# Optimization experiments

Hardware: AMD Instinct MI355X
Metric: run time of the kernel (lower is better)

## Reference

```python
import jax, jax.numpy as jnp
import numpy as np

B, I, O = 32768, 512, 512
EPS = 1e-5


def setup_inputs() -> dict:
    key = jax.random.key(0)
    ks = jax.random.split(key, 4)
    return {
        "input": jax.random.normal(ks[0], (B, I), dtype=jnp.float32),
        "h": jax.random.normal(ks[1], (B, O), dtype=jnp.float32),
        "c": jax.random.normal(ks[2], (B, O), dtype=jnp.float32),
        "W": jax.random.normal(ks[3], (4 * O, I + O), dtype=jnp.float32) * (1.0 / np.sqrt(I + O)),
        "gamma": jnp.ones((4, O), dtype=jnp.float32),
        "beta": jnp.zeros((4, O), dtype=jnp.float32),
    }


def reference(input, h, c, W, gamma, beta):
    # fused input projection: [B, I+O] @ [I+O, 4O] -> [B, 4, O]
    z = jnp.einsum("bi,gi->bg", jnp.concatenate([input, h], axis=-1), W)
    z = z.reshape(z.shape[0], 4, O)
    # LayerNorm over the trailing [4, O] dims jointly (torch LayerNorm([x, o_size]))
    mean = jnp.mean(z, axis=(-2, -1), keepdims=True)
    var = jnp.var(z, axis=(-2, -1), keepdims=True)
    zn = (z - mean) * jax.lax.rsqrt(var + EPS) * gamma + beta
    f_gate = jax.nn.sigmoid(zn[:, 0])
    i_gate = jax.nn.sigmoid(zn[:, 1])
    o_gate = jax.nn.sigmoid(zn[:, 2])
    # GELU (torch default = exact erf); dropout is identity in eval mode
    h_state = jax.nn.gelu(zn[:, 3], approximate=False)
    cell = f_gate * c + i_gate * h_state
    output = o_gate * cell
    return (output, cell)
```

## Files before the change

kernel.cpp:

```cpp
#include <hip/hip_runtime.h>
#include <hip/hip_bf16.h>
#include <cstdint>
#include <cstddef>

#define BDIM 32768
#define IDIM 512
#define ODIM 512
#define KDIM 1024
#define NDIM 2048

typedef __attribute__((ext_vector_type(8))) __bf16 bf16x8;
typedef __attribute__((ext_vector_type(4))) float f32x4;
typedef __attribute__((ext_vector_type(8))) unsigned short u16x8;

__device__ __forceinline__ unsigned short f2bf(float x) {
  union { float f; uint32_t u; } v; v.f = x;
  uint32_t r = v.u + 0x7FFFu + ((v.u >> 16) & 1u);
  return (unsigned short)(r >> 16);
}

__device__ __forceinline__ float bf2f(unsigned short s) {
  union { uint32_t u; float f; } v; v.u = ((uint32_t)s) << 16;
  return v.f;
}


__global__ __launch_bounds__(256) void pack_a_kernel(const float* __restrict__ in,
                                                     const float* __restrict__ h,
                                                     unsigned short* __restrict__ A) {
  size_t t = (size_t)blockIdx.x * 256 + threadIdx.x;
  size_t e = t * 8;
  size_t b = e >> 10;
  int col = (int)(e & 1023);
  const float* src = (col < IDIM) ? (in + b * IDIM + col)
                                  : (h + b * ODIM + (col - IDIM));
  float4 v0 = ((const float4*)src)[0];
  float4 v1 = ((const float4*)src)[1];
  u16x8 r;
  r[0] = f2bf(v0.x); r[1] = f2bf(v0.y); r[2] = f2bf(v0.z); r[3] = f2bf(v0.w);
  r[4] = f2bf(v1.x); r[5] = f2bf(v1.y); r[6] = f2bf(v1.z); r[7] = f2bf(v1.w);
  *(u16x8*)(A + e) = r;
}

__global__ __launch_bounds__(256) void pack_w_kernel(const float* __restrict__ Wsrc,
                                                     unsigned short* __restrict__ Wb) {
  size_t t = (size_t)blockIdx.x * 256 + threadIdx.x;
  size_t e = t * 8;
  float4 v0 = ((const float4*)(Wsrc + e))[0];
  float4 v1 = ((const float4*)(Wsrc + e))[1];
  u16x8 r;
  r[0] = f2bf(v0.x); r[1] = f2bf(v0.y); r[2] = f2bf(v0.z); r[3] = f2bf(v0.w);
  r[4] = f2bf(v1.x); r[5] = f2bf(v1.y); r[6] = f2bf(v1.z); r[7] = f2bf(v1.w);
  *(u16x8*)(Wb + e) = r;
}


#define GB 65536

#define BAR() do { asm volatile("" ::: "memory"); __builtin_amdgcn_s_barrier(); asm volatile("" ::: "memory"); } while (0)
#define VMW(n) asm volatile("s_waitcnt vmcnt(" #n ")" ::: "memory")
#define LGKM0() do { asm volatile("s_waitcnt lgkmcnt(0)" ::: "memory"); __builtin_amdgcn_sched_barrier(0); } while (0)

__device__ __forceinline__ void gll16(const unsigned short* src, char* ldsdst) {
  __builtin_amdgcn_global_load_lds(
      (const __attribute__((address_space(1))) void*)src,
      (__attribute__((address_space(3))) void*)ldsdst, 16, 0, 0);
}

__device__ __forceinline__ void mf16(const bf16x8 (&a)[4], const bf16x8 (&q)[4],
                                     f32x4 (&acc)[8][4], int mb) {
#pragma unroll
  for (int i = 0; i < 4; ++i)
#pragma unroll
    for (int j = 0; j < 4; ++j)
      acc[mb + i][j] = __builtin_amdgcn_mfma_f32_16x16x32_bf16(a[i], q[j], acc[mb + i][j], 0, 0, 0);
}

template<int BUF, bool STG, bool FINAL>
__device__ __forceinline__ void ktile(char* aR, char* bR, char* stA, char* stB,
                                      const unsigned short* pA0, const unsigned short* pA1,
                                      const unsigned short* pB0, const unsigned short* pB1,
                                      int stOff, f32x4 (&acc)[8][4]) {
  bf16x8 af[4], qf[4];
#pragma unroll
  for (int i = 0; i < 4; ++i) af[i] = *(const bf16x8*)(aR + i * 1024);
#pragma unroll
  for (int j = 0; j < 4; ++j) qf[j] = *(const bf16x8*)(bR + j * 1024);
  if (STG) { gll16(pA0, stA + stOff); gll16(pA1, stA + 8192 + stOff); }
  BAR(); LGKM0();
  __builtin_amdgcn_s_setprio(1);
  mf16(af, qf, acc, 0);
  __builtin_amdgcn_s_setprio(0);
  __builtin_amdgcn_sched_barrier(0);
  BAR();
#pragma unroll
  for (int i = 0; i < 4; ++i) af[i] = *(const bf16x8*)(aR + (4 + i) * 1024);
  if (STG) { gll16(pB0, stB + stOff); gll16(pB1, stB + 8192 + stOff); }
  BAR(); LGKM0();
  __builtin_amdgcn_s_setprio(1);
  mf16(af, qf, acc, 4);
  __builtin_amdgcn_s_setprio(0);
  __builtin_amdgcn_sched_barrier(0);
  if (FINAL) VMW(0); else VMW(4);
  BAR();
#pragma unroll
  for (int i = 0; i < 4; ++i) af[i] = *(const bf16x8*)(aR + 16384 + i * 1024);
#pragma unroll
  for (int j = 0; j < 4; ++j) qf[j] = *(const bf16x8*)(bR + 16384 + j * 1024);
  if (STG) { gll16(pA0 + 32, stA + 16384 + stOff); gll16(pA1 + 32, stA + 24576 + stOff); }
  BAR(); LGKM0();
  __builtin_amdgcn_s_setprio(1);
  mf16(af, qf, acc, 0);
  __builtin_amdgcn_s_setprio(0);
  __builtin_amdgcn_sched_barrier(0);
  BAR();
#pragma unroll
  for (int i = 0; i < 4; ++i) af[i] = *(const bf16x8*)(aR + 16384 + (4 + i) * 1024);
  if (STG) { gll16(pB0 + 32, stB + 16384 + stOff); gll16(pB1 + 32, stB + 24576 + stOff); }
  BAR(); LGKM0();
  __builtin_amdgcn_s_setprio(1);
  mf16(af, qf, acc, 4);
  __builtin_amdgcn_s_setprio(0);
  __builtin_amdgcn_sched_barrier(0);
  if (!FINAL) VMW(4);
  BAR();
}

__global__ __launch_bounds__(512, 2) void gemm_kernel(const unsigned short* __restrict__ A,
                                                      const unsigned short* __restrict__ Bt,
                                                      unsigned short* __restrict__ Cz) {
  extern __shared__ char smem[];
  const int tid = threadIdx.x;
  const int w = tid >> 6;
  const int lane = tid & 63;

  const int bid = blockIdx.x;
  const int swz = (bid & 7) * 128 + (bid >> 3);
  const int m0 = (swz >> 3) * 256;
  const int n0 = (swz & 7) * 256;

  const int wm = (w >> 2) * 128;
  const int wn = (w & 3) * 64;
  const int lrow = lane & 15;
  const int lk = (lane >> 4) * 8;

  char* aR0 = smem + (w >> 2) * 8192 + lane * 16;
  char* bR0 = smem + 32768 + (w & 3) * 4096 + lane * 16;
  char* aR1 = aR0 + GB;
  char* bR1 = bR0 + GB;
  const int stOff = w * 1024 + lane * 16;

  const unsigned short* pA0 = A  + (size_t)(m0 + w * 16       + lrow) * KDIM + lk;
  const unsigned short* pA1 = A  + (size_t)(m0 + (8 + w) * 16 + lrow) * KDIM + lk;
  const unsigned short* pB0 = Bt + (size_t)(n0 + w * 16       + lrow) * KDIM + lk;
  const unsigned short* pB1 = Bt + (size_t)(n0 + (8 + w) * 16 + lrow) * KDIM + lk;

  f32x4 acc[8][4] = {};

  gll16(pA0,      smem + stOff);
  gll16(pA1,      smem + 8192 + stOff);
  gll16(pB0,      smem + 32768 + stOff);
  gll16(pB1,      smem + 40960 + stOff);
  gll16(pA0 + 32, smem + 16384 + stOff);
  gll16(pA1 + 32, smem + 24576 + stOff);
  gll16(pB0 + 32, smem + 49152 + stOff);
  gll16(pB1 + 32, smem + 57344 + stOff);
  VMW(4);
  BAR();
  pA0 += 64; pA1 += 64; pB0 += 64; pB1 += 64;

  for (int tt = 0; tt < 7; ++tt) {
    ktile<0, true, false>(aR0, bR0, smem + GB, smem + GB + 32768, pA0, pA1, pB0, pB1, stOff, acc);
    pA0 += 64; pA1 += 64; pB0 += 64; pB1 += 64;
    ktile<1, true, false>(aR1, bR1, smem, smem + 32768, pA0, pA1, pB0, pB1, stOff, acc);
    pA0 += 64; pA1 += 64; pB0 += 64; pB1 += 64;
  }
  ktile<0, true, false>(aR0, bR0, smem + GB, smem + GB + 32768, pA0, pA1, pB0, pB1, stOff, acc);
  ktile<1, false, true>(aR1, bR1, smem, smem + 32768, pA0, pA1, pB0, pB1, stOff, acc);

#pragma unroll
  for (int mi = 0; mi < 8; ++mi) {
#pragma unroll
    for (int ni = 0; ni < 4; ++ni) {
#pragma unroll
      for (int r = 0; r < 4; ++r) {
        const int row = m0 + wm + mi * 16 + (lane >> 4) * 4 + r;
        const int col = n0 + wn + ni * 16 + lrow;
        Cz[(size_t)row * NDIM + col] = f2bf(acc[mi][ni][r]);
      }
    }
  }
}


__global__ __launch_bounds__(256) void ln_gate_kernel(const unsigned short* __restrict__ z,
                                                      const float* __restrict__ c,
                                                      const float* __restrict__ gamma,
                                                      const float* __restrict__ beta,
                                                      float* __restrict__ out) {
  __shared__ float rowbuf[4][NDIM];
  const int wave = threadIdx.x >> 6;
  const int lane = threadIdx.x & 63;
  const int row = blockIdx.x * 4 + wave;
  const unsigned short* zr = z + (size_t)row * NDIM;

  float s = 0.f, ss = 0.f;
#pragma unroll
  for (int j = 0; j < 4; ++j) {
    const int chunk = j * 64 + lane;
    u16x8 v = *(const u16x8*)(zr + chunk * 8);
    float f[8];
#pragma unroll
    for (int i2 = 0; i2 < 8; ++i2) {
      f[i2] = bf2f(v[i2]);
      s += f[i2];
      ss += f[i2] * f[i2];
    }
    float4* dst = (float4*)&rowbuf[wave][chunk * 8];
    dst[0] = make_float4(f[0], f[1], f[2], f[3]);
    dst[1] = make_float4(f[4], f[5], f[6], f[7]);
  }
#pragma unroll
  for (int off = 32; off > 0; off >>= 1) {
    s += __shfl_xor(s, off, 64);
    ss += __shfl_xor(ss, off, 64);
  }
  const float mean = s * (1.f / (float)NDIM);
  const float var = ss * (1.f / (float)NDIM) - mean * mean;
  const float inv = rsqrtf(var + 1e-5f);

  float* out_o = out + (size_t)row * ODIM;
  float* out_c = out + (size_t)BDIM * ODIM + (size_t)row * ODIM;
  const float* crow = c + (size_t)row * ODIM;

#pragma unroll
  for (int j = 0; j < 8; ++j) {
    const int o = j * 64 + lane;
    float zn[4];
#pragma unroll
    for (int g = 0; g < 4; ++g) {
      float v = (rowbuf[wave][g * ODIM + o] - mean) * inv;
      zn[g] = v * gamma[g * ODIM + o] + beta[g * ODIM + o];
    }
    const float fg = 1.f / (1.f + expf(-zn[0]));
    const float ig = 1.f / (1.f + expf(-zn[1]));
    const float og = 1.f / (1.f + expf(-zn[2]));
    const float x = zn[3];
    const float hs = 0.5f * x * (1.f + erff(x * 0.70710678118654752f));
    const float cc = fg * crow[o] + ig * hs;
    out_c[o] = cc;
    out_o[o] = og * cc;
  }
}


extern "C" void kernel_launch(void* const* d_in, const int* in_sizes, int n_in,
                              void* d_out, int out_size, void* d_ws, size_t ws_size,
                              hipStream_t stream) {
  const float* input = (const float*)d_in[0];
  const float* h     = (const float*)d_in[1];
  const float* c     = (const float*)d_in[2];
  const float* W     = (const float*)d_in[3];
  const float* gamma = (const float*)d_in[4];
  const float* beta  = (const float*)d_in[5];

  unsigned short* A  = (unsigned short*)d_ws;
  unsigned short* Wb = A + (size_t)BDIM * KDIM;
  unsigned short* z  = Wb + (size_t)NDIM * KDIM;
  float* out = (float*)d_out;

  hipFuncSetAttribute((const void*)gemm_kernel,
                      hipFuncAttributeMaxDynamicSharedMemorySize, 131072);

  pack_a_kernel<<<(BDIM * KDIM / 8) / 256, 256, 0, stream>>>(input, h, A);
  pack_w_kernel<<<(NDIM * KDIM / 8) / 256, 256, 0, stream>>>(W, Wb);
  gemm_kernel<<<dim3((BDIM / 256) * (NDIM / 256)), 512, 131072, stream>>>(A, Wb, z);
  ln_gate_kernel<<<BDIM / 4, 256, 0, stream>>>(z, c, gamma, beta, out);
}
```

Baseline: 284.0 us.

## Restructure GEMM main loop into a four-stage LDS ring with one barrier per k-step

Replaces the double-buffered, four-barrier-per-tile GEMM pipeline with a four-buffer ring of 32-deep k-slices, prefetching three stages ahead. Each k-step now waits on vmcnt, issues a single barrier, loads all A/B fragments, issues the next prefetch and runs 32 MFMAs. The aim is to cut barrier and lgkm wait overhead and deepen memory latency hiding. LDS use drops from 128KB to 128KB total across four 32KB buffers. There is only one barrier per step to guard reuse of the buffer being overwritten, which may race depending on ordering.

```diff
diff --git a/kernel.cpp b/kernel.cpp
--- a/kernel.cpp
+++ b/kernel.cpp
@@ -55,11 +55,10 @@
 }
 
 
-#define GB 65536
+#define BUFSZ 32768
 
 #define BAR() do { asm volatile("" ::: "memory"); __builtin_amdgcn_s_barrier(); asm volatile("" ::: "memory"); } while (0)
 #define VMW(n) asm volatile("s_waitcnt vmcnt(" #n ")" ::: "memory")
-#define LGKM0() do { asm volatile("s_waitcnt lgkmcnt(0)" ::: "memory"); __builtin_amdgcn_sched_barrier(0); } while (0)
 
 __device__ __forceinline__ void gll16(const unsigned short* src, char* ldsdst) {
   __builtin_amdgcn_global_load_lds(
@@ -67,63 +66,38 @@
       (__attribute__((address_space(3))) void*)ldsdst, 16, 0, 0);
 }
 
-__device__ __forceinline__ void mf16(const bf16x8 (&a)[4], const bf16x8 (&q)[4],
-                                     f32x4 (&acc)[8][4], int mb) {
-#pragma unroll
-  for (int i = 0; i < 4; ++i)
-#pragma unroll
-    for (int j = 0; j < 4; ++j)
-      acc[mb + i][j] = __builtin_amdgcn_mfma_f32_16x16x32_bf16(a[i], q[j], acc[mb + i][j], 0, 0, 0);
-}
-
-template<int BUF, bool STG, bool FINAL>
-__device__ __forceinline__ void ktile(char* aR, char* bR, char* stA, char* stB,
+template<int BUF, int VM, bool STG>
+__device__ __forceinline__ void ktile(char* smem, char* aR, char* bR,
                                       const unsigned short* pA0, const unsigned short* pA1,
                                       const unsigned short* pB0, const unsigned short* pB1,
                                       int stOff, f32x4 (&acc)[8][4]) {
-  bf16x8 af[4], qf[4];
-#pragma unroll
-  for (int i = 0; i < 4; ++i) af[i] = *(const bf16x8*)(aR + i * 1024);
-#pragma unroll
-  for (int j = 0; j < 4; ++j) qf[j] = *(const bf16x8*)(bR + j * 1024);
-  if (STG) { gll16(pA0, stA + stOff); gll16(pA1, stA + 8192 + stOff); }
-  BAR(); LGKM0();
+  constexpr int CB = BUF * BUFSZ;
+  constexpr int DB = ((BUF + 3) & 3) * BUFSZ;
+
+  if (VM == 8)      VMW(8);
+  else if (VM == 4) VMW(4);
+  else              VMW(0);
+  BAR();
+
+  bf16x8 af[8], qf[4];
+#pragma unroll
+  for (int i = 0; i < 8; ++i) af[i] = *(const bf16x8*)(aR + CB + i * 1024);
+#pragma unroll
+  for (int j = 0; j < 4; ++j) qf[j] = *(const bf16x8*)(bR + CB + j * 1024);
+  if (STG) {
+    gll16(pA0, smem + DB + stOff);
+    gll16(pA1, smem + DB + 8192 + stOff);
+    gll16(pB0, smem + DB + 16384 + stOff);
+    gll16(pB1, smem + DB + 24576 + stOff);
+  }
+  __builtin_amdgcn_sched_barrier(0);
   __builtin_amdgcn_s_setprio(1);
-  mf16(af, qf, acc, 0);
+#pragma unroll
+  for (int i = 0; i < 8; ++i)
+#pragma unroll
+    for (int j = 0; j < 4; ++j)
+      acc[i][j] = __builtin_amdgcn_mfma_f32_16x16x32_bf16(af[i], qf[j], acc[i][j], 0, 0, 0);
   __builtin_amdgcn_s_setprio(0);
-  __builtin_amdgcn_sched_barrier(0);
-  BAR();
-#pragma unroll
-  for (int i = 0; i < 4; ++i) af[i] = *(const bf16x8*)(aR + (4 + i) * 1024);
-  if (STG) { gll16(pB0, stB + stOff); gll16(pB1, stB + 8192 + stOff); }
-  BAR(); LGKM0();
-  __builtin_amdgcn_s_setprio(1);
-  mf16(af, qf, acc, 4);
-  __builtin_amdgcn_s_setprio(0);
-  __builtin_amdgcn_sched_barrier(0);
-  if (FINAL) VMW(0); else VMW(4);
-  BAR();
-#pragma unroll
-  for (int i = 0; i < 4; ++i) af[i] = *(const bf16x8*)(aR + 16384 + i * 1024);
-#pragma unroll
-  for (int j = 0; j < 4; ++j) qf[j] = *(const bf16x8*)(bR + 16384 + j * 1024);
-  if (STG) { gll16(pA0 + 32, stA + 16384 + stOff); gll16(pA1 + 32, stA + 24576 + stOff); }
-  BAR(); LGKM0();
-  __builtin_amdgcn_s_setprio(1);
-  mf16(af, qf, acc, 0);
-  __builtin_amdgcn_s_setprio(0);
-  __builtin_amdgcn_sched_barrier(0);
-  BAR();
-#pragma unroll
-  for (int i = 0; i < 4; ++i) af[i] = *(const bf16x8*)(aR + 16384 + (4 + i) * 1024);
-  if (STG) { gll16(pB0 + 32, stB + 16384 + stOff); gll16(pB1 + 32, stB + 24576 + stOff); }
-  BAR(); LGKM0();
-  __builtin_amdgcn_s_setprio(1);
-  mf16(af, qf, acc, 4);
-  __builtin_amdgcn_s_setprio(0);
-  __builtin_amdgcn_sched_barrier(0);
-  if (!FINAL) VMW(4);
-  BAR();
 }
 
 __global__ __launch_bounds__(512, 2) void gemm_kernel(const unsigned short* __restrict__ A,
@@ -144,10 +118,8 @@
   const int lrow = lane & 15;
   const int lk = (lane >> 4) * 8;
 
-  char* aR0 = smem + (w >> 2) * 8192 + lane * 16;
-  char* bR0 = smem + 32768 + (w & 3) * 4096 + lane * 16;
-  char* aR1 = aR0 + GB;
-  char* bR1 = bR0 + GB;
+  char* aR = smem + (w >> 2) * 8192 + lane * 16;
+  char* bR = smem + 16384 + (w & 3) * 4096 + lane * 16;
   const int stOff = w * 1024 + lane * 16;
 
   const unsigned short* pA0 = A  + (size_t)(m0 + w * 16       + lrow) * KDIM + lk;
@@ -157,26 +129,29 @@
 
   f32x4 acc[8][4] = {};
 
-  gll16(pA0,      smem + stOff);
-  gll16(pA1,      smem + 8192 + stOff);
-  gll16(pB0,      smem + 32768 + stOff);
-  gll16(pB1,      smem + 40960 + stOff);
-  gll16(pA0 + 32, smem + 16384 + stOff);
-  gll16(pA1 + 32, smem + 24576 + stOff);
-  gll16(pB0 + 32, smem + 49152 + stOff);
-  gll16(pB1 + 32, smem + 57344 + stOff);
-  VMW(4);
-  BAR();
-  pA0 += 64; pA1 += 64; pB0 += 64; pB1 += 64;
+#pragma unroll
+  for (int t = 0; t < 3; ++t) {
+    gll16(pA0 + t * 32, smem + t * BUFSZ + stOff);
+    gll16(pA1 + t * 32, smem + t * BUFSZ + 8192 + stOff);
+    gll16(pB0 + t * 32, smem + t * BUFSZ + 16384 + stOff);
+    gll16(pB1 + t * 32, smem + t * BUFSZ + 24576 + stOff);
+  }
+  pA0 += 96; pA1 += 96; pB0 += 96; pB1 += 96;
 
   for (int tt = 0; tt < 7; ++tt) {
-    ktile<0, true, false>(aR0, bR0, smem + GB, smem + GB + 32768, pA0, pA1, pB0, pB1, stOff, acc);
-    pA0 += 64; pA1 += 64; pB0 += 64; pB1 += 64;
-    ktile<1, true, false>(aR1, bR1, smem, smem + 32768, pA0, pA1, pB0, pB1, stOff, acc);
-    pA0 += 64; pA1 += 64; pB0 += 64; pB1 += 64;
-  }
-  ktile<0, true, false>(aR0, bR0, smem + GB, smem + GB + 32768, pA0, pA1, pB0, pB1, stOff, acc);
-  ktile<1, false, true>(aR1, bR1, smem, smem + 32768, pA0, pA1, pB0, pB1, stOff, acc);
+    ktile<0, 8, true>(smem, aR, bR, pA0, pA1, pB0, pB1, stOff, acc);
+    pA0 += 32; pA1 += 32; pB0 += 32; pB1 += 32;
+    ktile<1, 8, true>(smem, aR, bR, pA0, pA1, pB0, pB1, stOff, acc);
+    pA0 += 32; pA1 += 32; pB0 += 32; pB1 += 32;
+    ktile<2, 8, true>(smem, aR, bR, pA0, pA1, pB0, pB1, stOff, acc);
+    pA0 += 32; pA1 += 32; pB0 += 32; pB1 += 32;
+    ktile<3, 8, true>(smem, aR, bR, pA0, pA1, pB0, pB1, stOff, acc);
+    pA0 += 32; pA1 += 32; pB0 += 32; pB1 += 32;
+  }
+  ktile<0, 8, true >(smem, aR, bR, pA0, pA1, pB0, pB1, stOff, acc);
+  ktile<1, 8, false>(smem, aR, bR, pA0, pA1, pB0, pB1, stOff, acc);
+  ktile<2, 4, false>(smem, aR, bR, pA0, pA1, pB0, pB1, stOff, acc);
+  ktile<3, 0, false>(smem, aR, bR, pA0, pA1, pB0, pB1, stOff, acc);
 
 #pragma unroll
   for (int mi = 0; mi < 8; ++mi) {
```

After: 283.9 us. Within noise of the previous version (-0.0%).
